# Performance work log

Measured on AMD Instinct MI355X. Metric: run time of the kernel, lower is better.

## Reference

```python
import jax, jax.numpy as jnp
import numpy as np


def setup_inputs() -> dict:
    key = jax.random.key(0)
    ks = jax.random.split(key, 8)
    B, T, D, H, R = 64, 1024, 512, 512, 64
    s = lambda n: 1.0 / np.sqrt(n)
    return {
        "x":   jax.random.normal(ks[0], (B, T, D), jnp.float32),
        "W_w": jax.random.normal(ks[1], (4 * H, D), jnp.float32) * s(D),
        "W_b": jax.random.normal(ks[2], (4 * H,), jnp.float32) * 0.01,
        "U_w": jax.random.normal(ks[3], (4 * H, H), jnp.float32) * s(H),
        "U_b": jax.random.normal(ks[4], (4 * H,), jnp.float32) * 0.01,
        "A_w": jax.random.normal(ks[5], (R, D), jnp.float32) * s(D),
        "B_w": jax.random.normal(ks[6], (R, H), jnp.float32) * s(H),
        "P_w": jax.random.normal(ks[7], (H, R), jnp.float32) * s(R),
    }


def reference(x, W_w, W_b, U_w, U_b, A_w, B_w, P_w):
    # x: [B,T,D]. Dropout is identity (eval mode).
    Bsz, T, _ = x.shape
    H = U_w.shape[0] // 4
    # Precompute all input-side projections in parallel (no recurrence dep).
    Wx = jnp.einsum('btd,hd->bth', x, W_w) + W_b          # [B,T,4H]
    Ax = jnp.einsum('btd,rd->btr', x, A_w)                # [B,T,R]

    def step(carry, inp):
        h, c = carry
        wx_t, ax_t = inp                                  # [B,4H], [B,R]
        gates = wx_t + h @ U_w.T + U_b                    # [B,4H]
        i, f, o, g = jnp.split(gates, 4, axis=-1)
        i = jax.nn.sigmoid(i)
        f = jax.nn.sigmoid(f)
        o = jax.nn.sigmoid(o)
        g = jnp.tanh(g)
        mix = (ax_t * (h @ B_w.T)) @ P_w.T                # [B,H]
        c = f * c + i * g + 0.1 * mix
        h = o * jnp.tanh(c)
        return (h, c), h

    h0 = jnp.zeros((Bsz, H), x.dtype)
    c0 = jnp.zeros((Bsz, H), x.dtype)
    (h, c), outs = jax.lax.scan(
        step, (h0, c0),
        (jnp.swapaxes(Wx, 0, 1), jnp.swapaxes(Ax, 0, 1)))
    outs = jnp.swapaxes(outs, 0, 1)                       # [B,T,H]
    return outs, h, c
```

## Files before the change

### kernel.cpp

```cpp
#include <hip/hip_runtime.h>
#include <stdint.h>


typedef float    f32x4  __attribute__((ext_vector_type(4)));
typedef __bf16   bf16x8 __attribute__((ext_vector_type(8)));
typedef uint16_t u16;
typedef uint16_t u16x8  __attribute__((ext_vector_type(8)));
typedef uint32_t u32x4  __attribute__((ext_vector_type(4)));

#define WS_XB     0
#define WS_WC     67108864
#define WS_BIAS   69337088
#define WS_U      69345792
#define WS_BW     71442944
#define WS_P      71508480
#define WS_HBUF   71574016
#define WS_CNT    71705088
#define WS_WXC    71706112

#define OUT_H     33554432
#define OUT_C     33587200

__device__ __forceinline__ u16 f2bf(float f) {
  uint32_t u = __builtin_bit_cast(uint32_t, f);
  u = (u + 0x7fffu + ((u >> 16) & 1u)) >> 16;
  return (u16)u;
}
__device__ __forceinline__ float bf2f(u16 b) {
  uint32_t u = ((uint32_t)b) << 16;
  return __builtin_bit_cast(float, u);
}
__device__ __forceinline__ f32x4 mfma16(u16x8 a, u16x8 b, f32x4 c) {
  return __builtin_amdgcn_mfma_f32_16x16x32_bf16(
      __builtin_bit_cast(bf16x8, a), __builtin_bit_cast(bf16x8, b), c, 0, 0, 0);
}
__device__ __forceinline__ float sigm(float x) { return 1.f / (1.f + __expf(-x)); }
__device__ __forceinline__ float tanh_fast(float x) {
  float a = fabsf(x);
  float e = __expf(2.f * a);
  float t = 1.f - 2.f / (e + 1.f);
  return x < 0.f ? -t : t;
}

__global__ void cast_x(const float* __restrict__ x, u16* __restrict__ xb) {
  int i = blockIdx.x * 256 + threadIdx.x;
  const float4* src = (const float4*)x;
  float4 a = src[(size_t)i * 2];
  float4 b = src[(size_t)i * 2 + 1];
  u16x8 o;
  o[0] = f2bf(a.x); o[1] = f2bf(a.y); o[2] = f2bf(a.z); o[3] = f2bf(a.w);
  o[4] = f2bf(b.x); o[5] = f2bf(b.y); o[6] = f2bf(b.z); o[7] = f2bf(b.w);
  *(u16x8*)(xb + (size_t)i * 8) = o;
}

__global__ void prep(const float* __restrict__ W_w, const float* __restrict__ W_b,
                     const float* __restrict__ U_w, const float* __restrict__ U_b,
                     const float* __restrict__ A_w, const float* __restrict__ B_w,
                     const float* __restrict__ P_w,
                     u16* __restrict__ Wc, float* __restrict__ bias,
                     u16* __restrict__ Ubf, u16* __restrict__ Bwbf,
                     u16* __restrict__ Pbf, int* __restrict__ flags) {
  const int total = 1114112 + 1048576 + 32768 + 32768 + 2176 + 256;
  for (int i = blockIdx.x * blockDim.x + threadIdx.x; i < total;
       i += gridDim.x * blockDim.x) {
    int idx = i;
    if (idx < 1114112) {
      int row = idx >> 9, k = idx & 511;
      float v = 0.f;
      if (row < 2048) v = W_w[row * 512 + k];
      else if (row < 2112) v = A_w[(row - 2048) * 512 + k];
      Wc[idx] = f2bf(v);
      continue;
    }
    idx -= 1114112;
    if (idx < 1048576) { Ubf[idx] = f2bf(U_w[idx]); continue; }
    idx -= 1048576;
    if (idx < 32768) { Bwbf[idx] = f2bf(B_w[idx]); continue; }
    idx -= 32768;
    if (idx < 32768) { Pbf[idx] = f2bf(0.1f * P_w[idx]); continue; }
    idx -= 32768;
    if (idx < 2176) {
      bias[idx] = (idx < 2048) ? (W_b[idx] + U_b[idx]) : 0.f;
      continue;
    }
    idx -= 2176;
    flags[idx] = 0;
  }
}

__global__ void __launch_bounds__(256) gemm_wxc(const u16* __restrict__ xb,
                                                const u16* __restrict__ Wc,
                                                const float* __restrict__ bias,
                                                u16* __restrict__ outWx) {
  __shared__ u16 Atile[128 * 64];
  __shared__ u16 Btile[128 * 64];
  const int n0 = blockIdx.x * 128;
  const int m0 = blockIdx.y * 128;
  const int tid = threadIdx.x, ln = tid & 63, wv = tid >> 6;
  const int wm = (wv >> 1) * 64, wn = (wv & 1) * 64;
  f32x4 acc[4][4] = {};

  for (int k0 = 0; k0 < 512; k0 += 64) {
    __syncthreads();
    #pragma unroll
    for (int q = 0; q < 4; ++q) {
      int idx = tid + q * 256;
      int row = idx >> 3, kc = idx & 7;
      uint4 va = *(const uint4*)(xb + (size_t)(m0 + row) * 512 + k0 + kc * 8);
      *(uint4*)((char*)Atile + row * 128 + ((kc * 16) ^ ((row & 7) << 4))) = va;
      uint4 vb = *(const uint4*)(Wc + (size_t)(n0 + row) * 512 + k0 + kc * 8);
      *(uint4*)((char*)Btile + row * 128 + ((kc * 16) ^ ((row & 7) << 4))) = vb;
    }
    __syncthreads();
    #pragma unroll
    for (int kk = 0; kk < 64; kk += 32) {
      u16x8 af[4], bf[4];
      const int kb = kk * 2 + ((ln >> 4) << 4);
      #pragma unroll
      for (int i = 0; i < 4; ++i) {
        int arow = wm + i * 16 + (ln & 15);
        af[i] = *(const u16x8*)((char*)Atile + arow * 128 + (kb ^ ((arow & 7) << 4)));
        int brow = wn + i * 16 + (ln & 15);
        bf[i] = *(const u16x8*)((char*)Btile + brow * 128 + (kb ^ ((brow & 7) << 4)));
      }
      #pragma unroll
      for (int i = 0; i < 4; ++i)
        #pragma unroll
        for (int j = 0; j < 4; ++j)
          acc[i][j] = mfma16(af[i], bf[j], acc[i][j]);
    }
  }
  #pragma unroll
  for (int i = 0; i < 4; ++i) {
    const int mrow = m0 + wm + i * 16 + ((ln >> 4) << 2);
    #pragma unroll
    for (int j = 0; j < 4; ++j) {
      const int n = n0 + wn + j * 16 + (ln & 15);
      if (n < 2112) {
        const float bv = bias[n];
        #pragma unroll
        for (int r = 0; r < 4; ++r)
          outWx[(size_t)(mrow + r) * 2112 + n] = f2bf(acc[i][j][r] + bv);
      }
    }
  }
}

__global__ void __launch_bounds__(512, 2) recurrent(const u16* __restrict__ Wxc,
                                                    const u16* __restrict__ Ubf,
                                                    const u16* __restrict__ Bwbf,
                                                    const u16* __restrict__ Pbf,
                                                    u16* __restrict__ hbuf,
                                                    int* __restrict__ flagbuf,
                                                    float* __restrict__ out) {
  __shared__ char  h_lds[16 * 1024];
  __shared__ float v_buf[16 * 68];
  __shared__ float g_buf[4 * 16 * 17];

  const int tid = threadIdx.x;
  const int wv = tid >> 6, ln = tid & 63;
  const int grp = blockIdx.x & 3;
  const int ublk = blockIdx.x >> 2;
  const int u0 = ublk << 4, b0 = grp << 4;

  int* flags  = flagbuf + grp * 32;
  int* myflag = flags + ublk;

  u16x8 bfrag[16];
  {
    const u16* src = (wv < 4)
        ? (Ubf + (size_t)(wv * 512 + u0 + (ln & 15)) * 512)
        : (Bwbf + (size_t)((wv - 4) * 16 + (ln & 15)) * 512);
    #pragma unroll
    for (int ks = 0; ks < 16; ++ks)
      bfrag[ks] = *(const u16x8*)(src + ks * 32 + ((ln >> 4) << 3));
  }
  u16x8 pfrag[2];
  #pragma unroll
  for (int ks = 0; ks < 2; ++ks)
    pfrag[ks] = *(const u16x8*)(Pbf + (size_t)(u0 + (ln & 15)) * 64 + ks * 32 + ((ln >> 4) << 3));

  for (int i = tid; i < 1024; i += 512)
    ((u32x4*)h_lds)[i] = (u32x4){0u, 0u, 0u, 0u};
  __syncthreads();

  const int arow_base = (ln & 15) * 1024;
  const int a_xor = (ln & 7) << 4;
  const int a_k0 = (ln >> 4) << 4;

  uint32_t wx_cur[4] = {0, 0, 0, 0};
  u16x8 ax0_cur = {}, ax1_cur = {};
  {
    if (wv < 4) {
      const int col = wv * 512 + u0 + (ln & 15);
      const size_t rb = ((size_t)(b0 + ((ln >> 4) << 2)) * 1024 + 0) * 2112;
      #pragma unroll
      for (int j = 0; j < 4; ++j) wx_cur[j] = Wxc[rb + (size_t)j * 1024 * 2112 + col];
    }
    if (wv == 0) {
      const u16* axp = Wxc + ((size_t)(b0 + (ln & 15)) * 1024 + 0) * 2112 + 2048 + ((ln >> 4) << 3);
      ax0_cur = *(const u16x8*)(axp);
      ax1_cur = *(const u16x8*)(axp + 32);
    }
  }

  float c_reg[4] = {0.f, 0.f, 0.f, 0.f};
  float h_last[4] = {0.f, 0.f, 0.f, 0.f};

  #pragma unroll 1
  for (int t = 0; t < 1024; ++t) {
    f32x4 acc0 = {0.f, 0.f, 0.f, 0.f}, acc1 = {0.f, 0.f, 0.f, 0.f};
    #pragma unroll
    for (int ks = 0; ks < 16; ks += 2) {
      u16x8 a0 = *(const u16x8*)(h_lds + arow_base + ((ks * 64 + a_k0) ^ a_xor));
      u16x8 a1 = *(const u16x8*)(h_lds + arow_base + (((ks + 1) * 64 + a_k0) ^ a_xor));
      acc0 = mfma16(a0, bfrag[ks], acc0);
      acc1 = mfma16(a1, bfrag[ks + 1], acc1);
    }
    const f32x4 acc = acc0 + acc1;

    if (wv >= 4) {
      const int r = ((wv - 4) << 4) + (ln & 15);
      const int br = (ln >> 4) << 2;
      #pragma unroll
      for (int j = 0; j < 4; ++j) v_buf[(br + j) * 68 + r] = acc[j];
    } else {
      const int gi = wv * 272 + (ln & 15);
      const int br = (ln >> 4) << 2;
      #pragma unroll
      for (int j = 0; j < 4; ++j) {
        float g = acc[j] + bf2f((u16)wx_cur[j]);
        g = (wv == 3) ? tanh_fast(g) : sigm(g);
        g_buf[gi + (br + j) * 17] = g;
      }
    }
    __syncthreads();

    if (wv == 0) {
      __builtin_amdgcn_s_setprio(1);
      f32x4 accm = {0.f, 0.f, 0.f, 0.f};
      const int bb = ln & 15;
      const int r0 = (ln >> 4) << 3;
      u16x8 af;
      #pragma unroll
      for (int i = 0; i < 8; ++i)
        af[i] = f2bf(bf2f(ax0_cur[i]) * v_buf[bb * 68 + r0 + i]);
      accm = mfma16(af, pfrag[0], accm);
      #pragma unroll
      for (int i = 0; i < 8; ++i)
        af[i] = f2bf(bf2f(ax1_cur[i]) * v_buf[bb * 68 + 32 + r0 + i]);
      accm = mfma16(af, pfrag[1], accm);
      const int u = ln & 15;
      const int brb = (ln >> 4) * 4;
      u16* hdst = hbuf + (size_t)(t & 1) * 32768;
      float hv[4];
      #pragma unroll
      for (int j = 0; j < 4; ++j) {
        const int go = (brb + j) * 17 + u;
        float iv = g_buf[go];
        float fv = g_buf[272 + go];
        float ov = g_buf[544 + go];
        float gv = g_buf[816 + go];
        c_reg[j] = fv * c_reg[j] + iv * gv + accm[j];
        hv[j] = ov * tanh_fast(c_reg[j]);
        h_last[j] = hv[j];
        __hip_atomic_store(hdst + (size_t)(b0 + brb + j) * 512 + u0 + u,
                           f2bf(hv[j]), __ATOMIC_RELAXED, __HIP_MEMORY_SCOPE_AGENT);
      }
      asm volatile("s_waitcnt vmcnt(0)" ::: "memory");
      if (ln == 0)
        __hip_atomic_store(myflag, t + 1, __ATOMIC_RELAXED, __HIP_MEMORY_SCOPE_AGENT);
      __builtin_amdgcn_s_setprio(0);
      #pragma unroll
      for (int j = 0; j < 4; ++j)
        out[((size_t)(b0 + brb + j) * 1024 + t) * 512 + u0 + u] = hv[j];
    }

    {
      const int tn = (t < 1023) ? t + 1 : 1023;
      if (wv < 4 && wv != 1) {
        const int col = wv * 512 + u0 + (ln & 15);
        const size_t rb = ((size_t)(b0 + ((ln >> 4) << 2)) * 1024 + tn) * 2112;
        #pragma unroll
        for (int j = 0; j < 4; ++j) wx_cur[j] = Wxc[rb + (size_t)j * 1024 * 2112 + col];
      }
      if (wv == 0) {
        const u16* axp = Wxc + ((size_t)(b0 + (ln & 15)) * 1024 + tn) * 2112 + 2048 + ((ln >> 4) << 3);
        ax0_cur = *(const u16x8*)(axp);
        ax1_cur = *(const u16x8*)(axp + 32);
      }
    }

    if (wv == 1) {
      int* fp = flags + (ln & 31);
      const int target = t + 1;
      while (true) {
        int f = __hip_atomic_load(fp, __ATOMIC_RELAXED, __HIP_MEMORY_SCOPE_AGENT);
        if (__ballot(f >= target) == ~0ull) break;
      }
      if (t < 1023) {
        const int col = 512 + u0 + (ln & 15);
        const size_t rb = ((size_t)(b0 + ((ln >> 4) << 2)) * 1024 + t + 1) * 2112;
        #pragma unroll
        for (int j = 0; j < 4; ++j) wx_cur[j] = Wxc[rb + (size_t)j * 1024 * 2112 + col];
      }
    }
    __syncthreads();

    {
      const int row0 = tid >> 6, kc = tid & 63;
      const u16* base = hbuf + (size_t)(t & 1) * 32768 + (size_t)b0 * 512 + kc * 8;
      const u16* p0 = base + (size_t)row0 * 512;
      const u16* p1 = base + (size_t)(row0 + 8) * 512;
      u32x4 v0, v1;
      asm volatile(
          "global_load_dwordx4 %0, %2, off sc1\n\t"
          "global_load_dwordx4 %1, %3, off sc1\n\t"
          "s_waitcnt vmcnt(0)"
          : "=&v"(v0), "=&v"(v1)
          : "v"(p0), "v"(p1)
          : "memory");
      *(u32x4*)(h_lds + row0 * 1024 + ((kc * 16) ^ ((row0 & 7) << 4))) = v0;
      *(u32x4*)(h_lds + (row0 + 8) * 1024 + ((kc * 16) ^ (((row0 + 8) & 7) << 4))) = v1;
    }
    __syncthreads();
  }

  if (wv == 0) {
    const int u = ln & 15, brb = (ln >> 4) * 4;
    #pragma unroll
    for (int j = 0; j < 4; ++j) {
      out[OUT_H + (size_t)(b0 + brb + j) * 512 + u0 + u] = h_last[j];
      out[OUT_C + (size_t)(b0 + brb + j) * 512 + u0 + u] = c_reg[j];
    }
  }
}

extern "C" void kernel_launch(void* const* d_in, const int* in_sizes, int n_in,
                              void* d_out, int out_size, void* d_ws, size_t ws_size,
                              hipStream_t stream) {
  const float* x   = (const float*)d_in[0];
  const float* W_w = (const float*)d_in[1];
  const float* W_b = (const float*)d_in[2];
  const float* U_w = (const float*)d_in[3];
  const float* U_b = (const float*)d_in[4];
  const float* A_w = (const float*)d_in[5];
  const float* B_w = (const float*)d_in[6];
  const float* P_w = (const float*)d_in[7];
  char* ws = (char*)d_ws;

  u16*   xb   = (u16*)(ws + WS_XB);
  u16*   Wc   = (u16*)(ws + WS_WC);
  float* bias = (float*)(ws + WS_BIAS);
  u16*   Ubf  = (u16*)(ws + WS_U);
  u16*   Bwbf = (u16*)(ws + WS_BW);
  u16*   Pbf  = (u16*)(ws + WS_P);
  u16*   hbuf = (u16*)(ws + WS_HBUF);
  int*   flg  = (int*)(ws + WS_CNT);
  u16*   Wxc  = (u16*)(ws + WS_WXC);
  float* outp = (float*)d_out;

  cast_x<<<16384, 256, 0, stream>>>(x, xb);
  prep<<<2048, 256, 0, stream>>>(W_w, W_b, U_w, U_b, A_w, B_w, P_w,
                                 Wc, bias, Ubf, Bwbf, Pbf, flg);
  gemm_wxc<<<dim3(17, 512), 256, 0, stream>>>(xb, Wc, bias, Wxc);

  void* args[] = { &Wxc, &Ubf, &Bwbf, &Pbf, &hbuf, &flg, &outp };
  hipError_t e = hipLaunchCooperativeKernel((const void*)recurrent, dim3(128),
                                            dim3(512), args, 0, stream);
  if (e != hipSuccess) {
    recurrent<<<dim3(128), dim3(512), 0, stream>>>(Wxc, Ubf, Bwbf, Pbf,
                                                   hbuf, flg, outp);
  }
}
```

Before: 4.317 ms.

## Replace flag-based inter-block sync with tagged h values polled directly

Removes the separate per-block flag counters and the store-wait-flag sequence. Each h value is now published as a 32-bit word holding a step tag in the high half and the bf16 value in the low half, written as coalesced 16-byte stores through an LDS staging buffer. All waves poll the h buffer itself until every tag matches the step, then unpack into LDS. This cuts one full barrier and a flag round trip per timestep, in exchange for doubling the bytes of h traffic and having every wave spin on global loads. Plain __syncthreads is also swapped for a cheaper LDS-only barrier.

```diff
diff --git a/kernel.cpp b/kernel.cpp
--- a/kernel.cpp
+++ b/kernel.cpp
@@ -6,6 +6,7 @@
 typedef __bf16   bf16x8 __attribute__((ext_vector_type(8)));
 typedef uint16_t u16;
 typedef uint16_t u16x8  __attribute__((ext_vector_type(8)));
+typedef uint32_t u32x2  __attribute__((ext_vector_type(2)));
 typedef uint32_t u32x4  __attribute__((ext_vector_type(4)));
 
 #define WS_XB     0
@@ -14,9 +15,8 @@
 #define WS_U      69345792
 #define WS_BW     71442944
 #define WS_P      71508480
-#define WS_HBUF   71574016
-#define WS_CNT    71705088
-#define WS_WXC    71706112
+#define WS_HPACK  71574016
+#define WS_WXC    71836160
 
 #define OUT_H     33554432
 #define OUT_C     33587200
@@ -40,6 +40,12 @@
   float e = __expf(2.f * a);
   float t = 1.f - 2.f / (e + 1.f);
   return x < 0.f ? -t : t;
+}
+__device__ __forceinline__ void lds_barrier() {
+  asm volatile("s_waitcnt lgkmcnt(0)" ::: "memory");
+  __builtin_amdgcn_sched_barrier(0);
+  __builtin_amdgcn_s_barrier();
+  __builtin_amdgcn_sched_barrier(0);
 }
 
 __global__ void cast_x(const float* __restrict__ x, u16* __restrict__ xb) {
@@ -59,8 +65,8 @@
                      const float* __restrict__ P_w,
                      u16* __restrict__ Wc, float* __restrict__ bias,
                      u16* __restrict__ Ubf, u16* __restrict__ Bwbf,
-                     u16* __restrict__ Pbf, int* __restrict__ flags) {
-  const int total = 1114112 + 1048576 + 32768 + 32768 + 2176 + 256;
+                     u16* __restrict__ Pbf, uint32_t* __restrict__ hpack) {
+  const int total = 1114112 + 1048576 + 32768 + 32768 + 2176 + 65536;
   for (int i = blockIdx.x * blockDim.x + threadIdx.x; i < total;
        i += gridDim.x * blockDim.x) {
     int idx = i;
@@ -84,7 +90,7 @@
       continue;
     }
     idx -= 2176;
-    flags[idx] = 0;
+    hpack[idx] = 0;
   }
 }
 
@@ -150,12 +156,12 @@
                                                     const u16* __restrict__ Ubf,
                                                     const u16* __restrict__ Bwbf,
                                                     const u16* __restrict__ Pbf,
-                                                    u16* __restrict__ hbuf,
-                                                    int* __restrict__ flagbuf,
+                                                    uint32_t* __restrict__ hpack,
                                                     float* __restrict__ out) {
-  __shared__ char  h_lds[16 * 1024];
-  __shared__ float v_buf[16 * 68];
-  __shared__ float g_buf[4 * 16 * 17];
+  __shared__ char     h_lds[16 * 1024];
+  __shared__ float    v_buf[16 * 68];
+  __shared__ float    g_buf[4 * 16 * 17];
+  __shared__ uint32_t hpub[16 * 16];
 
   const int tid = threadIdx.x;
   const int wv = tid >> 6, ln = tid & 63;
@@ -163,9 +169,6 @@
   const int ublk = blockIdx.x >> 2;
   const int u0 = ublk << 4, b0 = grp << 4;
 
-  int* flags  = flagbuf + grp * 32;
-  int* myflag = flags + ublk;
-
   u16x8 bfrag[16];
   {
     const u16* src = (wv < 4)
@@ -188,14 +191,18 @@
   const int a_xor = (ln & 7) << 4;
   const int a_k0 = (ln >> 4) << 4;
 
+  const int rb = tid >> 7;
+  const int cs = (tid & 127) * 4;
+  const int lbyte = (tid & 127) * 8;
+
   uint32_t wx_cur[4] = {0, 0, 0, 0};
   u16x8 ax0_cur = {}, ax1_cur = {};
   {
     if (wv < 4) {
       const int col = wv * 512 + u0 + (ln & 15);
-      const size_t rb = ((size_t)(b0 + ((ln >> 4) << 2)) * 1024 + 0) * 2112;
-      #pragma unroll
-      for (int j = 0; j < 4; ++j) wx_cur[j] = Wxc[rb + (size_t)j * 1024 * 2112 + col];
+      const size_t rbase = ((size_t)(b0 + ((ln >> 4) << 2)) * 1024 + 0) * 2112;
+      #pragma unroll
+      for (int j = 0; j < 4; ++j) wx_cur[j] = Wxc[rbase + (size_t)j * 1024 * 2112 + col];
     }
     if (wv == 0) {
       const u16* axp = Wxc + ((size_t)(b0 + (ln & 15)) * 1024 + 0) * 2112 + 2048 + ((ln >> 4) << 3);
@@ -234,7 +241,7 @@
         g_buf[gi + (br + j) * 17] = g;
       }
     }
-    __syncthreads();
+    lds_barrier();
 
     if (wv == 0) {
       __builtin_amdgcn_s_setprio(1);
@@ -252,7 +259,6 @@
       accm = mfma16(af, pfrag[1], accm);
       const int u = ln & 15;
       const int brb = (ln >> 4) * 4;
-      u16* hdst = hbuf + (size_t)(t & 1) * 32768;
       float hv[4];
       #pragma unroll
       for (int j = 0; j < 4; ++j) {
@@ -264,66 +270,74 @@
         c_reg[j] = fv * c_reg[j] + iv * gv + accm[j];
         hv[j] = ov * tanh_fast(c_reg[j]);
         h_last[j] = hv[j];
-        __hip_atomic_store(hdst + (size_t)(b0 + brb + j) * 512 + u0 + u,
-                           f2bf(hv[j]), __ATOMIC_RELAXED, __HIP_MEMORY_SCOPE_AGENT);
-      }
-      asm volatile("s_waitcnt vmcnt(0)" ::: "memory");
-      if (ln == 0)
-        __hip_atomic_store(myflag, t + 1, __ATOMIC_RELAXED, __HIP_MEMORY_SCOPE_AGENT);
+        out[((size_t)(b0 + brb + j) * 1024 + t) * 512 + u0 + u] = hv[j];
+      }
+      if (t < 1023) {
+        const uint32_t tagv = ((uint32_t)(t + 1)) << 16;
+        #pragma unroll
+        for (int j = 0; j < 4; ++j)
+          hpub[(brb + j) * 16 + u] = tagv | (uint32_t)f2bf(hv[j]);
+        asm volatile("s_waitcnt lgkmcnt(0)" ::: "memory");
+        __builtin_amdgcn_sched_barrier(0);
+        u32x4 pv = *(const u32x4*)&hpub[(ln >> 2) * 16 + (ln & 3) * 4];
+        uint32_t* dst = hpack + (size_t)((t & 1) ? 32768 : 0)
+                        + (size_t)(b0 + (ln >> 2)) * 512 + u0 + (ln & 3) * 4;
+        asm volatile("global_store_dwordx4 %0, %1, off sc1"
+                     :: "v"(dst), "v"(pv) : "memory");
+      }
       __builtin_amdgcn_s_setprio(0);
-      #pragma unroll
-      for (int j = 0; j < 4; ++j)
-        out[((size_t)(b0 + brb + j) * 1024 + t) * 512 + u0 + u] = hv[j];
-    }
-
-    {
-      const int tn = (t < 1023) ? t + 1 : 1023;
-      if (wv < 4 && wv != 1) {
+    }
+
+    if (t < 1023) {
+      const uint32_t tg = (uint32_t)(t + 1);
+      uint32_t* hb = hpack + (size_t)((t & 1) ? 32768 : 0) + (size_t)b0 * 512;
+      const uint32_t* p0 = hb + (size_t)(rb)*512 + cs;
+      const uint32_t* p1 = hb + (size_t)(rb + 4) * 512 + cs;
+      const uint32_t* p2 = hb + (size_t)(rb + 8) * 512 + cs;
+      const uint32_t* p3 = hb + (size_t)(rb + 12) * 512 + cs;
+      u32x4 A, B, C, D;
+      while (true) {
+        asm volatile(
+            "global_load_dwordx4 %0, %4, off sc1\n\t"
+            "global_load_dwordx4 %1, %5, off sc1\n\t"
+            "global_load_dwordx4 %2, %6, off sc1\n\t"
+            "global_load_dwordx4 %3, %7, off sc1\n\t"
+            "s_waitcnt vmcnt(0)"
+            : "=&v"(A), "=&v"(B), "=&v"(C), "=&v"(D)
+            : "v"(p0), "v"(p1), "v"(p2), "v"(p3)
+            : "memory");
+        bool ok = (A[0] >> 16) >= tg && (A[1] >> 16) >= tg &&
+                  (A[2] >> 16) >= tg && (A[3] >> 16) >= tg &&
+                  (B[0] >> 16) >= tg && (B[1] >> 16) >= tg &&
+                  (B[2] >> 16) >= tg && (B[3] >> 16) >= tg &&
+                  (C[0] >> 16) >= tg && (C[1] >> 16) >= tg &&
+                  (C[2] >> 16) >= tg && (C[3] >> 16) >= tg &&
+                  (D[0] >> 16) >= tg && (D[1] >> 16) >= tg &&
+                  (D[2] >> 16) >= tg && (D[3] >> 16) >= tg;
+        if (__ballot(ok) == ~0ull) break;
+      }
+      if (wv < 4) {
         const int col = wv * 512 + u0 + (ln & 15);
-        const size_t rb = ((size_t)(b0 + ((ln >> 4) << 2)) * 1024 + tn) * 2112;
+        const size_t rbase = ((size_t)(b0 + ((ln >> 4) << 2)) * 1024 + t + 1) * 2112;
         #pragma unroll
-        for (int j = 0; j < 4; ++j) wx_cur[j] = Wxc[rb + (size_t)j * 1024 * 2112 + col];
+        for (int j = 0; j < 4; ++j) wx_cur[j] = Wxc[rbase + (size_t)j * 1024 * 2112 + col];
       }
       if (wv == 0) {
-        const u16* axp = Wxc + ((size_t)(b0 + (ln & 15)) * 1024 + tn) * 2112 + 2048 + ((ln >> 4) << 3);
+        const u16* axp = Wxc + ((size_t)(b0 + (ln & 15)) * 1024 + t + 1) * 2112 + 2048 + ((ln >> 4) << 3);
         ax0_cur = *(const u16x8*)(axp);
         ax1_cur = *(const u16x8*)(axp + 32);
       }
-    }
-
-    if (wv == 1) {
-      int* fp = flags + (ln & 31);
-      const int target = t + 1;
-      while (true) {
-        int f = __hip_atomic_load(fp, __ATOMIC_RELAXED, __HIP_MEMORY_SCOPE_AGENT);
-        if (__ballot(f >= target) == ~0ull) break;
-      }
-      if (t < 1023) {
-        const int col = 512 + u0 + (ln & 15);
-        const size_t rb = ((size_t)(b0 + ((ln >> 4) << 2)) * 1024 + t + 1) * 2112;
-        #pragma unroll
-        for (int j = 0; j < 4; ++j) wx_cur[j] = Wxc[rb + (size_t)j * 1024 * 2112 + col];
-      }
-    }
-    __syncthreads();
-
-    {
-      const int row0 = tid >> 6, kc = tid & 63;
-      const u16* base = hbuf + (size_t)(t & 1) * 32768 + (size_t)b0 * 512 + kc * 8;
-      const u16* p0 = base + (size_t)row0 * 512;
-      const u16* p1 = base + (size_t)(row0 + 8) * 512;
-      u32x4 v0, v1;
-      asm volatile(
-          "global_load_dwordx4 %0, %2, off sc1\n\t"
-          "global_load_dwordx4 %1, %3, off sc1\n\t"
-          "s_waitcnt vmcnt(0)"
-          : "=&v"(v0), "=&v"(v1)
-          : "v"(p0), "v"(p1)
-          : "memory");
-      *(u32x4*)(h_lds + row0 * 1024 + ((kc * 16) ^ ((row0 & 7) << 4))) = v0;
-      *(u32x4*)(h_lds + (row0 + 8) * 1024 + ((kc * 16) ^ (((row0 + 8) & 7) << 4))) = v1;
-    }
-    __syncthreads();
+      #pragma unroll
+      for (int k = 0; k < 4; ++k) {
+        const int r = rb + 4 * k;
+        u32x4 v = (k == 0) ? A : (k == 1) ? B : (k == 2) ? C : D;
+        u32x2 w;
+        w[0] = (v[0] & 0xffffu) | (v[1] << 16);
+        w[1] = (v[2] & 0xffffu) | (v[3] << 16);
+        *(u32x2*)(h_lds + r * 1024 + (lbyte ^ ((r & 7) << 4))) = w;
+      }
+    }
+    lds_barrier();
   }
 
   if (wv == 0) {
@@ -349,27 +363,26 @@
   const float* P_w = (const float*)d_in[7];
   char* ws = (char*)d_ws;
 
-  u16*   xb   = (u16*)(ws + WS_XB);
-  u16*   Wc   = (u16*)(ws + WS_WC);
-  float* bias = (float*)(ws + WS_BIAS);
-  u16*   Ubf  = (u16*)(ws + WS_U);
-  u16*   Bwbf = (u16*)(ws + WS_BW);
-  u16*   Pbf  = (u16*)(ws + WS_P);
-  u16*   hbuf = (u16*)(ws + WS_HBUF);
-  int*   flg  = (int*)(ws + WS_CNT);
-  u16*   Wxc  = (u16*)(ws + WS_WXC);
-  float* outp = (float*)d_out;
+  u16*      xb    = (u16*)(ws + WS_XB);
+  u16*      Wc    = (u16*)(ws + WS_WC);
+  float*    bias  = (float*)(ws + WS_BIAS);
+  u16*      Ubf   = (u16*)(ws + WS_U);
+  u16*      Bwbf  = (u16*)(ws + WS_BW);
+  u16*      Pbf   = (u16*)(ws + WS_P);
+  uint32_t* hpack = (uint32_t*)(ws + WS_HPACK);
+  u16*      Wxc   = (u16*)(ws + WS_WXC);
+  float*    outp  = (float*)d_out;
 
   cast_x<<<16384, 256, 0, stream>>>(x, xb);
   prep<<<2048, 256, 0, stream>>>(W_w, W_b, U_w, U_b, A_w, B_w, P_w,
-                                 Wc, bias, Ubf, Bwbf, Pbf, flg);
+                                 Wc, bias, Ubf, Bwbf, Pbf, hpack);
   gemm_wxc<<<dim3(17, 512), 256, 0, stream>>>(xb, Wc, bias, Wxc);
 
-  void* args[] = { &Wxc, &Ubf, &Bwbf, &Pbf, &hbuf, &flg, &outp };
+  void* args[] = { &Wxc, &Ubf, &Bwbf, &Pbf, &hpack, &outp };
   hipError_t e = hipLaunchCooperativeKernel((const void*)recurrent, dim3(128),
                                             dim3(512), args, 0, stream);
   if (e != hipSuccess) {
     recurrent<<<dim3(128), dim3(512), 0, stream>>>(Wxc, Ubf, Bwbf, Pbf,
-                                                   hbuf, flg, outp);
-  }
-}
+                                                   hpack, outp);
+  }
+}
```

Result: slower. 4.983 ms (+15.4%).

## Replace shared flag array with per-block mailbox lines and lighter LDS barriers

Applied to the files above, without the earlier changes.

Each producer block now writes its step counter into a dedicated 32-entry mailbox line for every consumer block in its group. Consumers poll their own line instead of all polling the same shared flag words, which is meant to cut contention on the inter-block handoff inside the recurrent loop. __syncthreads is replaced by a raw s_barrier that waits only on LDS counters, and the next-step Wx/Ax prefetch is reorganised so each wave loads only its own data inside mutually exclusive branches. This costs 32x more flag stores per step from wave 0 and relies on hand-placed waitcnt being correct for the global loads that cross the barrier.

```diff
diff --git a/kernel.cpp b/kernel.cpp
--- a/kernel.cpp
+++ b/kernel.cpp
@@ -15,8 +15,8 @@
 #define WS_BW     71442944
 #define WS_P      71508480
 #define WS_HBUF   71574016
-#define WS_CNT    71705088
-#define WS_WXC    71706112
+#define WS_MBOX   71705088
+#define WS_WXC    71721472
 
 #define OUT_H     33554432
 #define OUT_C     33587200
@@ -40,6 +40,12 @@
   float e = __expf(2.f * a);
   float t = 1.f - 2.f / (e + 1.f);
   return x < 0.f ? -t : t;
+}
+__device__ __forceinline__ void lds_barrier() {
+  asm volatile("s_waitcnt lgkmcnt(0)" ::: "memory");
+  __builtin_amdgcn_sched_barrier(0);
+  __builtin_amdgcn_s_barrier();
+  __builtin_amdgcn_sched_barrier(0);
 }
 
 __global__ void cast_x(const float* __restrict__ x, u16* __restrict__ xb) {
@@ -59,8 +65,8 @@
                      const float* __restrict__ P_w,
                      u16* __restrict__ Wc, float* __restrict__ bias,
                      u16* __restrict__ Ubf, u16* __restrict__ Bwbf,
-                     u16* __restrict__ Pbf, int* __restrict__ flags) {
-  const int total = 1114112 + 1048576 + 32768 + 32768 + 2176 + 256;
+                     u16* __restrict__ Pbf, uint32_t* __restrict__ mbox) {
+  const int total = 1114112 + 1048576 + 32768 + 32768 + 2176 + 4096;
   for (int i = blockIdx.x * blockDim.x + threadIdx.x; i < total;
        i += gridDim.x * blockDim.x) {
     int idx = i;
@@ -84,7 +90,7 @@
       continue;
     }
     idx -= 2176;
-    flags[idx] = 0;
+    mbox[idx] = 0;
   }
 }
 
@@ -151,7 +157,7 @@
                                                     const u16* __restrict__ Bwbf,
                                                     const u16* __restrict__ Pbf,
                                                     u16* __restrict__ hbuf,
-                                                    int* __restrict__ flagbuf,
+                                                    uint32_t* __restrict__ mbox,
                                                     float* __restrict__ out) {
   __shared__ char  h_lds[16 * 1024];
   __shared__ float v_buf[16 * 68];
@@ -163,8 +169,8 @@
   const int ublk = blockIdx.x >> 2;
   const int u0 = ublk << 4, b0 = grp << 4;
 
-  int* flags  = flagbuf + grp * 32;
-  int* myflag = flags + ublk;
+  uint32_t* mb_grp = mbox + grp * 32 * 32;
+  uint32_t* my_line = mb_grp + ublk * 32;
 
   u16x8 bfrag[16];
   {
@@ -234,7 +240,7 @@
         g_buf[gi + (br + j) * 17] = g;
       }
     }
-    __syncthreads();
+    lds_barrier();
 
     if (wv == 0) {
       __builtin_amdgcn_s_setprio(1);
@@ -268,44 +274,43 @@
                            f2bf(hv[j]), __ATOMIC_RELAXED, __HIP_MEMORY_SCOPE_AGENT);
       }
       asm volatile("s_waitcnt vmcnt(0)" ::: "memory");
-      if (ln == 0)
-        __hip_atomic_store(myflag, t + 1, __ATOMIC_RELAXED, __HIP_MEMORY_SCOPE_AGENT);
+      if (ln < 32)
+        __hip_atomic_store(mb_grp + ln * 32 + ublk, (uint32_t)(t + 1),
+                           __ATOMIC_RELAXED, __HIP_MEMORY_SCOPE_AGENT);
       __builtin_amdgcn_s_setprio(0);
       #pragma unroll
       for (int j = 0; j < 4; ++j)
         out[((size_t)(b0 + brb + j) * 1024 + t) * 512 + u0 + u] = hv[j];
-    }
-
-    {
-      const int tn = (t < 1023) ? t + 1 : 1023;
-      if (wv < 4 && wv != 1) {
-        const int col = wv * 512 + u0 + (ln & 15);
+      {
+        const int tn = (t < 1023) ? t + 1 : 1023;
+        const u16* axp = Wxc + ((size_t)(b0 + (ln & 15)) * 1024 + tn) * 2112 + 2048 + ((ln >> 4) << 3);
+        ax0_cur = *(const u16x8*)(axp);
+        ax1_cur = *(const u16x8*)(axp + 32);
+        const int col = u0 + (ln & 15);
         const size_t rb = ((size_t)(b0 + ((ln >> 4) << 2)) * 1024 + tn) * 2112;
         #pragma unroll
         for (int j = 0; j < 4; ++j) wx_cur[j] = Wxc[rb + (size_t)j * 1024 * 2112 + col];
       }
-      if (wv == 0) {
-        const u16* axp = Wxc + ((size_t)(b0 + (ln & 15)) * 1024 + tn) * 2112 + 2048 + ((ln >> 4) << 3);
-        ax0_cur = *(const u16x8*)(axp);
-        ax1_cur = *(const u16x8*)(axp + 32);
-      }
-    }
-
-    if (wv == 1) {
-      int* fp = flags + (ln & 31);
-      const int target = t + 1;
+    } else if (wv == 1) {
+      uint32_t* fp = my_line + (ln & 31);
+      const uint32_t target = (uint32_t)(t + 1);
       while (true) {
-        int f = __hip_atomic_load(fp, __ATOMIC_RELAXED, __HIP_MEMORY_SCOPE_AGENT);
+        uint32_t f = __hip_atomic_load(fp, __ATOMIC_RELAXED, __HIP_MEMORY_SCOPE_AGENT);
         if (__ballot(f >= target) == ~0ull) break;
       }
-      if (t < 1023) {
-        const int col = 512 + u0 + (ln & 15);
-        const size_t rb = ((size_t)(b0 + ((ln >> 4) << 2)) * 1024 + t + 1) * 2112;
-        #pragma unroll
-        for (int j = 0; j < 4; ++j) wx_cur[j] = Wxc[rb + (size_t)j * 1024 * 2112 + col];
-      }
-    }
-    __syncthreads();
+      const int tn = (t < 1023) ? t + 1 : 1023;
+      const int col = 512 + u0 + (ln & 15);
+      const size_t rb = ((size_t)(b0 + ((ln >> 4) << 2)) * 1024 + tn) * 2112;
+      #pragma unroll
+      for (int j = 0; j < 4; ++j) wx_cur[j] = Wxc[rb + (size_t)j * 1024 * 2112 + col];
+    } else if (wv < 4) {
+      const int tn = (t < 1023) ? t + 1 : 1023;
+      const int col = wv * 512 + u0 + (ln & 15);
+      const size_t rb = ((size_t)(b0 + ((ln >> 4) << 2)) * 1024 + tn) * 2112;
+      #pragma unroll
+      for (int j = 0; j < 4; ++j) wx_cur[j] = Wxc[rb + (size_t)j * 1024 * 2112 + col];
+    }
+    lds_barrier();
 
     {
       const int row0 = tid >> 6, kc = tid & 63;
@@ -323,7 +328,7 @@
       *(u32x4*)(h_lds + row0 * 1024 + ((kc * 16) ^ ((row0 & 7) << 4))) = v0;
       *(u32x4*)(h_lds + (row0 + 8) * 1024 + ((kc * 16) ^ (((row0 + 8) & 7) << 4))) = v1;
     }
-    __syncthreads();
+    lds_barrier();
   }
 
   if (wv == 0) {
@@ -349,27 +354,27 @@
   const float* P_w = (const float*)d_in[7];
   char* ws = (char*)d_ws;
 
-  u16*   xb   = (u16*)(ws + WS_XB);
-  u16*   Wc   = (u16*)(ws + WS_WC);
-  float* bias = (float*)(ws + WS_BIAS);
-  u16*   Ubf  = (u16*)(ws + WS_U);
-  u16*   Bwbf = (u16*)(ws + WS_BW);
-  u16*   Pbf  = (u16*)(ws + WS_P);
-  u16*   hbuf = (u16*)(ws + WS_HBUF);
-  int*   flg  = (int*)(ws + WS_CNT);
-  u16*   Wxc  = (u16*)(ws + WS_WXC);
-  float* outp = (float*)d_out;
+  u16*      xb   = (u16*)(ws + WS_XB);
+  u16*      Wc   = (u16*)(ws + WS_WC);
+  float*    bias = (float*)(ws + WS_BIAS);
+  u16*      Ubf  = (u16*)(ws + WS_U);
+  u16*      Bwbf = (u16*)(ws + WS_BW);
+  u16*      Pbf  = (u16*)(ws + WS_P);
+  u16*      hbuf = (u16*)(ws + WS_HBUF);
+  uint32_t* mbox = (uint32_t*)(ws + WS_MBOX);
+  u16*      Wxc  = (u16*)(ws + WS_WXC);
+  float*    outp = (float*)d_out;
 
   cast_x<<<16384, 256, 0, stream>>>(x, xb);
   prep<<<2048, 256, 0, stream>>>(W_w, W_b, U_w, U_b, A_w, B_w, P_w,
-                                 Wc, bias, Ubf, Bwbf, Pbf, flg);
+                                 Wc, bias, Ubf, Bwbf, Pbf, mbox);
   gemm_wxc<<<dim3(17, 512), 256, 0, stream>>>(xb, Wc, bias, Wxc);
 
-  void* args[] = { &Wxc, &Ubf, &Bwbf, &Pbf, &hbuf, &flg, &outp };
+  void* args[] = { &Wxc, &Ubf, &Bwbf, &Pbf, &hbuf, &mbox, &outp };
   hipError_t e = hipLaunchCooperativeKernel((const void*)recurrent, dim3(128),
                                             dim3(512), args, 0, stream);
   if (e != hipSuccess) {
     recurrent<<<dim3(128), dim3(512), 0, stream>>>(Wxc, Ubf, Bwbf, Pbf,
-                                                   hbuf, flg, outp);
-  }
-}
+                                                   hbuf, mbox, outp);
+  }
+}
```

After: 3.885 ms (median of 2 runs). 1.11x faster.
